# Kernel tuning notes

Measured on AMD Instinct MI355X. Metric: run time of the kernel, lower is better.

The kernel has to match this reference:

```python
import jax, jax.numpy as jnp
import numpy as np

MEM, KEY, VAL, DIN, BS, BQ = 1000, 64, 128, 512, 512, 65536


def setup_inputs() -> dict:
    key = jax.random.key(0)
    ks = jax.random.split(key, 20)

    def lin(k, fan_in, shape):
        return (jax.random.normal(k, shape, jnp.float32) / np.sqrt(fan_in)).astype(jnp.float32)

    return {
        "support_x": jax.random.normal(ks[0], (BS, DIN), jnp.float32),
        "support_y": jax.random.normal(ks[1], (BS, VAL), jnp.float32),
        "query_x": jax.random.normal(ks[2], (BQ, DIN), jnp.float32),
        "query_y": jax.random.normal(ks[3], (BQ, 1), jnp.float32),
        # base model: Linear(DIN -> KEY)
        "base_W": lin(ks[4], DIN, (DIN, KEY)),
        "base_b": jnp.zeros((KEY,), jnp.float32),
        # ExternalMemory projections
        "kp_W": lin(ks[5], KEY, (KEY, KEY)),
        "kp_b": jnp.zeros((KEY,), jnp.float32),
        "vp_W": lin(ks[6], VAL, (VAL, VAL)),
        "vp_b": jnp.zeros((VAL,), jnp.float32),
        # memory buffers (randn keys/values like register_buffer(torch.randn))
        "mem_keys": jax.random.normal(ks[7], (MEM, KEY), jnp.float32),
        "mem_values": jax.random.normal(ks[8], (MEM, VAL), jnp.float32),
        # ages: uniform so top-k picks distinct slots deterministically
        "mem_age": jax.random.uniform(ks[9], (MEM,), jnp.float32),
        # controller MLP: Linear(KEY+VAL,128) ReLU Linear(128,64) ReLU Linear(64,1)
        "c1_W": lin(ks[10], KEY + VAL, (KEY + VAL, 128)),
        "c1_b": jnp.zeros((128,), jnp.float32),
        "c2_W": lin(ks[11], 128, (128, 64)),
        "c2_b": jnp.zeros((64,), jnp.float32),
        "c3_W": lin(ks[12], 64, (64, 1)),
        "c3_b": jnp.zeros((1,), jnp.float32),
    }


def reference(support_x, support_y, query_x, query_y,
              base_W, base_b, kp_W, kp_b, vp_W, vp_b,
              mem_keys, mem_values, mem_age,
              c1_W, c1_b, c2_W, c2_b, c3_W, c3_b):
    # base model features
    support_feat = support_x @ base_W + base_b          # [BS, KEY]
    query_feat = query_x @ base_W + base_b              # [BQ, KEY]

    # --- memory.write(support_feat, support_y) ---
    proj_keys = support_feat @ kp_W + kp_b              # [BS, KEY]
    proj_vals = support_y @ vp_W + vp_b                 # [BS, VAL]
    _, oldest = jax.lax.top_k(mem_age, BS)              # evict oldest BS slots
    new_keys = mem_keys.at[oldest].set(proj_keys)       # [MEM, KEY]
    new_values = mem_values.at[oldest].set(proj_vals)   # [MEM, VAL]

    # --- memory.read(query_feat) ---
    proj_q = query_feat @ kp_W + kp_b                   # [BQ, KEY]
    sims = proj_q @ new_keys.T                          # [BQ, MEM]
    attn = jax.nn.softmax(sims, axis=-1)
    retrieved = attn @ new_values                       # [BQ, VAL]

    # --- controller MLP on [query_feat ; retrieved] ---
    aug = jnp.concatenate([query_feat, retrieved], axis=-1)  # [BQ, KEY+VAL]
    h = jax.nn.relu(aug @ c1_W + c1_b)
    h = jax.nn.relu(h @ c2_W + c2_b)
    query_pred = h @ c3_W + c3_b                        # [BQ, 1]

    meta_loss = jnp.mean((query_pred - query_y) ** 2)
    return meta_loss, query_pred, retrieved
```

## Files before the change

### kernel.cpp

```cpp
#include <hip/hip_runtime.h>

typedef _Float16 h8v __attribute__((ext_vector_type(8)));
typedef _Float16 h4v __attribute__((ext_vector_type(4)));
typedef float    f4v __attribute__((ext_vector_type(4)));

#define MFMA16(a,b,c) __builtin_amdgcn_mfma_f32_16x16x32_f16((a),(b),(c),0,0,0)
#define NEGF (-1e30f)

#define MEM 1000
#define KEY 64
#define VAL 128
#define DIN 512
#define BS  512
#define BQ  65536
#define NCOPY 8


typedef __attribute__((address_space(1))) const unsigned int guint;
typedef __attribute__((address_space(3))) unsigned int luint;

__device__ __forceinline__ void gld16(const _Float16* g, _Float16* l)
{
  __builtin_amdgcn_global_load_lds((guint*)g, (luint*)l, 16, 0, 0);
}

__device__ __forceinline__ h8v cvt8(const float* p)
{
  f4v u = *(const f4v*)p;
  f4v v = *(const f4v*)(p + 4);
  h8v a;
  a[0] = (_Float16)u.x; a[1] = (_Float16)u.y; a[2] = (_Float16)u.z; a[3] = (_Float16)u.w;
  a[4] = (_Float16)v.x; a[5] = (_Float16)v.y; a[6] = (_Float16)v.z; a[7] = (_Float16)v.w;
  return a;
}

__device__ __forceinline__ h8v cvt8nt(const float* p)
{
  f4v u = __builtin_nontemporal_load((const f4v*)p);
  f4v v = __builtin_nontemporal_load((const f4v*)(p + 4));
  h8v a;
  a[0] = (_Float16)u.x; a[1] = (_Float16)u.y; a[2] = (_Float16)u.z; a[3] = (_Float16)u.w;
  a[4] = (_Float16)v.x; a[5] = (_Float16)v.y; a[6] = (_Float16)v.z; a[7] = (_Float16)v.w;
  return a;
}

__global__ void k_prep1(const float* __restrict__ baseW, const float* __restrict__ base_b,
                        const float* __restrict__ kpW, const float* __restrict__ kp_b,
                        const float* __restrict__ vpW, const float* __restrict__ c1W,
                        const float* __restrict__ c2W, const float* __restrict__ age,
                        _Float16* __restrict__ WTf, float* __restrict__ bcomb,
                        _Float16* __restrict__ vpWt, _Float16* __restrict__ c1F,
                        _Float16* __restrict__ c2F, int* __restrict__ ranks,
                        float* __restrict__ out0)
{
  long id = (long)blockIdx.x * 256 + threadIdx.x;
  if (id < 65536) {
    int h = (int)id;
    int j = h & 7, lane = (h >> 3) & 63, KS = (h >> 9) & 15, F = h >> 13;
    int n = F * 16 + (lane & 15);
    int k = KS * 32 + ((lane >> 4) << 3) + j;
    float v;
    if (n < 64) v = baseW[(size_t)k * 64 + n];
    else {
      int nn = n - 64;
      const float* br = baseW + (size_t)k * 64;
      float s = 0.f;
      for (int t = 0; t < 64; ++t) s += br[t] * kpW[t * 64 + nn];
      v = s;
    }
    WTf[h] = (_Float16)v;
  } else if (id < 65664) {
    int i = (int)(id - 65536);
    if (i < 64) bcomb[i] = base_b[i];
    else {
      int n = i - 64;
      float s = kp_b[n];
      for (int t = 0; t < 64; ++t) s += base_b[t] * kpW[t * 64 + n];
      bcomb[i] = s;
    }
  } else if (id < 90240) {
    int h = (int)(id - 65664);
    int j = h & 7, lane = (h >> 3) & 63, KS = (h >> 9) % 6, F = (h >> 9) / 6;
    int n = F * 16 + (lane & 15);
    int k = KS * 32 + ((lane >> 4) << 3) + j;
    c1F[h] = (_Float16)c1W[(size_t)k * 128 + n];
  } else if (id < 98432) {
    int h = (int)(id - 90240);
    int j = h & 7, lane = (h >> 3) & 63, KS = (h >> 9) & 3, F = h >> 11;
    int n = F * 16 + (lane & 15);
    int k = KS * 32 + ((lane >> 4) << 3) + j;
    c2F[h] = (_Float16)c2W[(size_t)k * 64 + n];
  } else if (id < 114816) {
    long i = id - 98432;
    int n = (int)(i >> 7), k = (int)(i & 127);
    vpWt[i] = (_Float16)vpW[(size_t)k * 128 + n];
  } else if (id < 115816) {
    int jx = (int)(id - 114816);
    float aj = age[jx];
    int r = 0;
    for (int i2 = 0; i2 < MEM; ++i2) {
      float ai = age[i2];
      r += (ai > aj) || (ai == aj && i2 < jx);
    }
    ranks[jx] = r;
  } else if (id == 115816) {
    *out0 = 0.f;
  }
}

__global__ __launch_bounds__(64) void k_prep2(
    const float* __restrict__ sx, const float* __restrict__ sy,
    const _Float16* __restrict__ WTf, const float* __restrict__ bcomb,
    const _Float16* __restrict__ vpWt, const float* __restrict__ vp_b,
    float* __restrict__ pkeys, float* __restrict__ pvals)
{
  const int lane = threadIdx.x, quad = lane >> 4, l15 = lane & 15;
  const f4v fz = {0.f, 0.f, 0.f, 0.f};
  if (blockIdx.x < 32) {
    const int m0 = blockIdx.x * 16;
    f4v acc[4];
    #pragma unroll
    for (int f = 0; f < 4; ++f) acc[f] = fz;
    const float* xr = sx + (size_t)(m0 + l15) * DIN;
    #pragma unroll 4
    for (int ks = 0; ks < 16; ++ks) {
      int k0 = ks * 32 + quad * 8;
      h8v a = cvt8(xr + k0);
      #pragma unroll
      for (int f = 0; f < 4; ++f) {
        h8v b = *(const h8v*)(WTf + (size_t)((((4 + f) * 16) + ks) * 64 + lane) * 8);
        acc[f] = MFMA16(a, b, acc[f]);
      }
    }
    #pragma unroll
    for (int f = 0; f < 4; ++f) {
      int col = f * 16 + l15;
      float bb = bcomb[64 + col];
      #pragma unroll
      for (int r = 0; r < 4; ++r)
        pkeys[(size_t)(m0 + quad * 4 + r) * KEY + col] = acc[f][r] + bb;
    }
  } else {
    const int m0 = (blockIdx.x - 32) * 16;
    f4v acc[8];
    #pragma unroll
    for (int f = 0; f < 8; ++f) acc[f] = fz;
    const float* yr = sy + (size_t)(m0 + l15) * VAL;
    #pragma unroll
    for (int ks = 0; ks < 4; ++ks) {
      int k0 = ks * 32 + quad * 8;
      h8v a = cvt8(yr + k0);
      #pragma unroll
      for (int f = 0; f < 8; ++f) {
        h8v b = *(const h8v*)(vpWt + (size_t)(f * 16 + l15) * 128 + k0);
        acc[f] = MFMA16(a, b, acc[f]);
      }
    }
    #pragma unroll
    for (int f = 0; f < 8; ++f) {
      int col = f * 16 + l15;
      float bb = vp_b[col];
      #pragma unroll
      for (int r = 0; r < 4; ++r)
        pvals[(size_t)(m0 + quad * 4 + r) * VAL + col] = acc[f][r] + bb;
    }
  }
}

__global__ void k_prep3(const int* __restrict__ ranks, const float* __restrict__ pk,
                        const float* __restrict__ pv, const float* __restrict__ memK,
                        const float* __restrict__ memV,
                        _Float16* __restrict__ keysF, _Float16* __restrict__ valF,
                        _Float16* __restrict__ WTf, _Float16* __restrict__ c1F,
                        _Float16* __restrict__ c2F)
{
  long id = (long)blockIdx.x * 256 + threadIdx.x;
  if (id < 8L * 65536) {
    int h = (int)(id & 65535);
    int copy = (int)(id >> 16);
    int j = h & 7, lane = (h >> 3) & 63, KS = (h >> 9) & 1, F = h >> 10;
    int n = F * 16 + (lane & 15);
    int k = KS * 32 + ((lane >> 4) << 3) + j;
    float v = 0.f;
    if (n < MEM) {
      int rk = ranks[n];
      v = (rk < BS) ? pk[(size_t)rk * KEY + k] : memK[(size_t)n * KEY + k];
    }
    keysF[(size_t)copy * 65536 + h] = (_Float16)v;
  } else if (id < 8L * 65536 + 8L * 131072) {
    long i = id - 8L * 65536;
    int h = (int)(i & 131071);
    int copy = (int)(i >> 17);
    int j = h & 7, lane = (h >> 3) & 63, KS = (h >> 9) & 31, F = h >> 14;
    int nv = F * 16 + (lane & 15);
    int jm = KS * 32 + ((j >> 2) << 4) + ((lane >> 4) << 2) + (j & 3);
    float v = 0.f;
    if (jm < MEM) {
      int rk = ranks[jm];
      v = (rk < BS) ? pv[(size_t)rk * VAL + nv] : memV[(size_t)jm * VAL + nv];
    }
    valF[(size_t)copy * 131072 + h] = (_Float16)v;
  } else {
    long i = id - (8L * 65536 + 8L * 131072);
    if (i < 7L * 65536) {
      int copy = 1 + (int)(i >> 16); int h = (int)(i & 65535);
      WTf[(size_t)copy * 65536 + h] = WTf[h];
    } else if ((i -= 7L * 65536) < 7L * 24576) {
      int copy = 1 + (int)(i / 24576); int h = (int)(i % 24576);
      c1F[(size_t)copy * 24576 + h] = c1F[h];
    } else if ((i -= 7L * 24576) < 7L * 8192) {
      int copy = 1 + (int)(i >> 13); int h = (int)(i & 8191);
      c2F[(size_t)copy * 8192 + h] = c2F[h];
    }
  }
}

__global__ __launch_bounds__(512, 4) void k_fused(
    const float* __restrict__ qx, const float* __restrict__ qy,
    const _Float16* __restrict__ WTf_, const float* __restrict__ bcomb,
    const float* __restrict__ c1_b, const float* __restrict__ c2_b,
    const float* __restrict__ c3W, const float* __restrict__ c3b,
    const _Float16* __restrict__ c1F_, const _Float16* __restrict__ c2F_,
    const _Float16* __restrict__ keysF_, const _Float16* __restrict__ valF_,
    float* __restrict__ dout)
{
  __shared__ __align__(16) char smem[65536];
  _Float16* const Wq0 = (_Float16*)smem;
  _Float16* const Wq1 = (_Float16*)(smem + 32768);
  _Float16* const K0 = (_Float16*)smem;
  _Float16* const K1 = (_Float16*)(smem + 8192);
  _Float16* const V0 = (_Float16*)(smem + 16384);
  _Float16* const V1 = (_Float16*)(smem + 32768);

  const int tid  = threadIdx.x;
  const int wid  = tid >> 6;
  const int lane = tid & 63;
  const int quad = lane >> 4;
  const int l15  = lane & 15;

  const int cpy  = blockIdx.x & 7;
  const int rot  = (blockIdx.x >> 3) & 15;
  const int qrot = (blockIdx.x >> 1) & 3;
  const _Float16* const WTf   = WTf_   + (size_t)cpy * 65536;
  const _Float16* const c1F   = c1F_   + (size_t)cpy * 24576;
  const _Float16* const c2F   = c2F_   + (size_t)cpy * 8192;
  const _Float16* const keysF = keysF_ + (size_t)cpy * 65536;
  const _Float16* const valF  = valF_  + (size_t)cpy * 131072;

  _Float16* const qstash = (_Float16*)(smem + 49152 + wid * 2048);
  _Float16* const P_s  = (_Float16*)(smem + wid * 6656);
  _Float16* const h2_s = P_s + 2176;

  const int tile = blockIdx.x * 8 + wid;
  const int q0   = tile * 16;

  float* out_pred = dout + 1;
  float* out_ret  = dout + 1 + BQ;
  const f4v fz = {0.f, 0.f, 0.f, 0.f};

  #pragma unroll
  for (int i = 0; i < 4; ++i) {
    const int t = wid * 4 + i;
    const int f = t >> 2, ksq = t & 3;
    gld16(WTf + (size_t)(f * 16 + qrot * 4 + ksq) * 512 + lane * 8, Wq0 + t * 512);
  }
  asm volatile("s_waitcnt vmcnt(0)" ::: "memory");
  __syncthreads();

  f4v acc[8];
  #pragma unroll
  for (int f = 0; f < 8; ++f) acc[f] = fz;
  const float* xr = qx + (size_t)(q0 + l15) * DIN;

  #pragma unroll
  for (int q = 0; q < 4; ++q) {
    const int qe = (q + qrot) & 3;
    _Float16* const Wb = (q & 1) ? Wq1 : Wq0;
    _Float16* const Wn = (q & 1) ? Wq0 : Wq1;
    if (q < 3) {
      const int qn = (q + 1 + qrot) & 3;
      #pragma unroll
      for (int i = 0; i < 4; ++i) {
        const int t = wid * 4 + i;
        const int f = t >> 2, ksq = t & 3;
        gld16(WTf + (size_t)(f * 16 + qn * 4 + ksq) * 512 + lane * 8,
              Wn + t * 512);
      }
    }
    #pragma unroll
    for (int ksq = 0; ksq < 4; ++ksq) {
      const int ks = qe * 4 + ksq;
      h8v a = cvt8nt(xr + ks * 32 + quad * 8);
      #pragma unroll
      for (int f = 0; f < 8; ++f) {
        h8v b = *(const h8v*)(Wb + (size_t)((f * 4 + ksq) * 64 + lane) * 8);
        acc[f] = MFMA16(a, b, acc[f]);
      }
    }
    asm volatile("s_waitcnt vmcnt(0)" ::: "memory");
    __syncthreads();
  }

  _Float16* tbuf = (_Float16*)(smem + wid * 4352);
  h8v pq0, pq1;
  {
    #pragma unroll
    for (int f = 0; f < 8; ++f) {
      float bb = bcomb[f * 16 + l15];
      #pragma unroll
      for (int r = 0; r < 4; ++r)
        tbuf[(quad * 4 + r) * 136 + f * 16 + l15] = (_Float16)(acc[f][r] + bb);
    }
    h8v qf0 = *(const h8v*)&tbuf[l15 * 136 +  0 + quad * 8];
    h8v qf1 = *(const h8v*)&tbuf[l15 * 136 + 32 + quad * 8];
    pq0 = *(const h8v*)&tbuf[l15 * 136 + 64 + quad * 8];
    pq1 = *(const h8v*)&tbuf[l15 * 136 + 96 + quad * 8];
    *(h8v*)&qstash[0 * 512 + lane * 8] = qf0;
    *(h8v*)&qstash[1 * 512 + lane * 8] = qf1;
  }
  __syncthreads();

  #pragma unroll
  for (int i = 0; i < 3; ++i) {
    const int t = wid * 3 + i;
    if (t < 8) gld16(keysF + (size_t)(rot * 8 + t) * 512 + lane * 8, K0 + t * 512);
    else {
      const int tv = t - 8;
      gld16(valF + (size_t)((tv >> 1) * 32 + rot * 2 + (tv & 1)) * 512 + lane * 8,
            V0 + tv * 512);
    }
  }
  asm volatile("s_waitcnt vmcnt(0)" ::: "memory");
  __syncthreads();

  float rm = NEGF, rl = 0.f;
  f4v O[8];
  #pragma unroll
  for (int v = 0; v < 8; ++v) O[v] = fz;

  #pragma unroll 1
  for (int c = 0; c < 16; ++c) {
    const int ce  = (c + rot) & 15;
    const int cur = c & 1;
    _Float16* const Kc = cur ? K1 : K0;
    _Float16* const Vc = cur ? V1 : V0;
    _Float16* const Kn = cur ? K0 : K1;
    _Float16* const Vn = cur ? V0 : V1;

    if (c < 15) {
      const int ne = (c + 1 + rot) & 15;
      #pragma unroll
      for (int i = 0; i < 3; ++i) {
        const int t = wid * 3 + i;
        if (t < 8)
          gld16(keysF + (size_t)(ne * 8 + t) * 512 + lane * 8, Kn + t * 512);
        else {
          const int tv = t - 8;
          gld16(valF + (size_t)((tv >> 1) * 32 + ne * 2 + (tv & 1)) * 512 + lane * 8,
                Vn + tv * 512);
        }
      }
    }

    f4v S[4];
    #pragma unroll
    for (int f = 0; f < 4; ++f) S[f] = fz;
    #pragma unroll
    for (int f = 0; f < 4; ++f) {
      h8v b0 = *(const h8v*)(Kc + (size_t)(f * 2 + 0) * 512 + lane * 8);
      h8v b1 = *(const h8v*)(Kc + (size_t)(f * 2 + 1) * 512 + lane * 8);
      S[f] = MFMA16(b0, pq0, S[f]);
      S[f] = MFMA16(b1, pq1, S[f]);
    }

    float cm = NEGF;
    #pragma unroll
    for (int f = 0; f < 4; ++f) {
      const int sb = ce * 64 + f * 16 + quad * 4;
      #pragma unroll
      for (int r = 0; r < 4; ++r) {
        float s = (sb + r < MEM) ? S[f][r] : NEGF;
        S[f][r] = s;
        cm = fmaxf(cm, s);
      }
    }
    cm = fmaxf(cm, __shfl_xor(cm, 16));
    cm = fmaxf(cm, __shfl_xor(cm, 32));
    if (__any(cm > rm)) {
      float mn = fmaxf(rm, cm);
      float al = __expf(rm - mn);
      rm = mn;
      float alO[4];
      #pragma unroll
      for (int r = 0; r < 4; ++r) alO[r] = __shfl(al, quad * 4 + r);
      #pragma unroll
      for (int v = 0; v < 8; ++v)
        #pragma unroll
        for (int r = 0; r < 4; ++r) O[v][r] *= alO[r];
      rl *= al;
    }
    float psl = 0.f;
    #pragma unroll
    for (int f = 0; f < 4; ++f)
      #pragma unroll
      for (int r = 0; r < 4; ++r) {
        float p = __expf(S[f][r] - rm);
        S[f][r] = p;
        psl += p;
      }
    rl += psl;

    #pragma unroll
    for (int ks2 = 0; ks2 < 2; ++ks2) {
      h8v a;
      #pragma unroll
      for (int e = 0; e < 4; ++e) {
        a[e]     = (_Float16)S[2 * ks2][e];
        a[e + 4] = (_Float16)S[2 * ks2 + 1][e];
      }
      #pragma unroll
      for (int v = 0; v < 8; ++v) {
        h8v b = *(const h8v*)(Vc + (size_t)(v * 2 + ks2) * 512 + lane * 8);
        O[v] = MFMA16(a, b, O[v]);
      }
    }

    asm volatile("s_waitcnt vmcnt(0)" ::: "memory");
    __syncthreads();
  }

  rl += __shfl_xor(rl, 16); rl += __shfl_xor(rl, 32);
  float rlO[4];
  #pragma unroll
  for (int r = 0; r < 4; ++r) rlO[r] = __shfl(rl, quad * 4 + r);

  h8v qf0 = *(const h8v*)&qstash[0 * 512 + lane * 8];
  h8v qf1 = *(const h8v*)&qstash[1 * 512 + lane * 8];
  __syncthreads();

  #pragma unroll
  for (int v = 0; v < 8; ++v)
    #pragma unroll
    for (int r = 0; r < 4; ++r)
      P_s[(quad * 4 + r) * 136 + v * 16 + l15] = (_Float16)(O[v][r] / rlO[r]);

  #pragma unroll
  for (int it = 0; it < 8; ++it) {
    int flat = it * 256 + lane * 4;
    int row = flat >> 7, col = flat & 127;
    h4v t = *(const h4v*)&P_s[row * 136 + col];
    f4v o;
    o.x = (float)t[0]; o.y = (float)t[1]; o.z = (float)t[2]; o.w = (float)t[3];
    __builtin_nontemporal_store(o, (f4v*)(out_ret + (size_t)q0 * VAL + flat));
  }

  {
    f4v H[8];
    #pragma unroll
    for (int f = 0; f < 8; ++f) H[f] = fz;
    #pragma unroll
    for (int ks = 0; ks < 6; ++ks) {
      const int k0 = ks * 32;
      h8v a = (ks == 0) ? qf0 : (ks == 1) ? qf1
               : *(const h8v*)&P_s[l15 * 136 + (k0 - 64) + quad * 8];
      #pragma unroll
      for (int f = 0; f < 8; ++f) {
        h8v b = *(const h8v*)(c1F + (size_t)(f * 6 + ks) * 512 + lane * 8);
        H[f] = MFMA16(a, b, H[f]);
      }
    }
    #pragma unroll
    for (int f = 0; f < 8; ++f) {
      float bb = c1_b[f * 16 + l15];
      #pragma unroll
      for (int r = 0; r < 4; ++r)
        P_s[(quad * 4 + r) * 136 + f * 16 + l15] =
            (_Float16)fmaxf(0.f, H[f][r] + bb);
    }
  }

  {
    f4v G[4];
    #pragma unroll
    for (int f = 0; f < 4; ++f) G[f] = fz;
    #pragma unroll
    for (int ks = 0; ks < 4; ++ks) {
      h8v a = *(const h8v*)&P_s[l15 * 136 + ks * 32 + quad * 8];
      #pragma unroll
      for (int f = 0; f < 4; ++f) {
        h8v b = *(const h8v*)(c2F + (size_t)(f * 4 + ks) * 512 + lane * 8);
        G[f] = MFMA16(a, b, G[f]);
      }
    }
    #pragma unroll
    for (int f = 0; f < 4; ++f) {
      float bb = c2_b[f * 16 + l15];
      #pragma unroll
      for (int r = 0; r < 4; ++r)
        h2_s[(quad * 4 + r) * 72 + f * 16 + l15] =
            (_Float16)fmaxf(0.f, G[f][r] + bb);
    }
  }

  float lsum;
  {
    const int prow = lane >> 2, pj = lane & 3;
    float s = 0.f;
    #pragma unroll
    for (int k = 0; k < 16; ++k) {
      int kk = pj * 16 + k;
      s += (float)h2_s[prow * 72 + kk] * c3W[kk];
    }
    s += __shfl_xor(s, 1);
    s += __shfl_xor(s, 2);
    float pred = s + c3b[0];
    float diff = pred - qy[q0 + prow];
    if (pj == 0) out_pred[q0 + prow] = pred;
    lsum = diff * diff;
  }
  #pragma unroll
  for (int m = 1; m < 64; m <<= 1) lsum += __shfl_xor(lsum, m);
  if (lane == 0) atomicAdd(dout, lsum * (1.0f / (4.0f * (float)BQ)));
}

extern "C" void kernel_launch(void* const* d_in, const int* in_sizes, int n_in,
                              void* d_out, int out_size, void* d_ws, size_t ws_size,
                              hipStream_t stream)
{
  const float* support_x = (const float*)d_in[0];
  const float* support_y = (const float*)d_in[1];
  const float* query_x   = (const float*)d_in[2];
  const float* query_y   = (const float*)d_in[3];
  const float* base_W    = (const float*)d_in[4];
  const float* base_b    = (const float*)d_in[5];
  const float* kp_W      = (const float*)d_in[6];
  const float* kp_b      = (const float*)d_in[7];
  const float* vp_W      = (const float*)d_in[8];
  const float* vp_b      = (const float*)d_in[9];
  const float* mem_keys  = (const float*)d_in[10];
  const float* mem_vals  = (const float*)d_in[11];
  const float* mem_age   = (const float*)d_in[12];
  const float* c1_W      = (const float*)d_in[13];
  const float* c1_b      = (const float*)d_in[14];
  const float* c2_W      = (const float*)d_in[15];
  const float* c2_b      = (const float*)d_in[16];
  const float* c3_W      = (const float*)d_in[17];
  const float* c3_b      = (const float*)d_in[18];

  char* w = (char*)d_ws;
  _Float16* WTf   = (_Float16*)(w + 0);
  _Float16* c1F   = (_Float16*)(w + 1048576);
  _Float16* c2F   = (_Float16*)(w + 1441792);
  _Float16* keysF = (_Float16*)(w + 1572864);
  _Float16* valF  = (_Float16*)(w + 2621440);
  _Float16* vpWt  = (_Float16*)(w + 4718592);
  float*    bcomb = (float*)   (w + 4751360);
  int*      ranks = (int*)     (w + 4751872);
  float*    pkeys = (float*)   (w + 4755968);
  float*    pvals = (float*)   (w + 4887040);

  float* out = (float*)d_out;

  hipLaunchKernelGGL(k_prep1, dim3(453), dim3(256), 0, stream,
                     base_W, base_b, kp_W, kp_b, vp_W, c1_W, c2_W, mem_age,
                     WTf, bcomb, vpWt, c1F, c2F, ranks, out);
  hipLaunchKernelGGL(k_prep2, dim3(64), dim3(64), 0, stream,
                     support_x, support_y, WTf, bcomb, vpWt, vp_b, pkeys, pvals);
  hipLaunchKernelGGL(k_prep3, dim3(8832), dim3(256), 0, stream,
                     ranks, pkeys, pvals, mem_keys, mem_vals, keysF, valF,
                     WTf, c1F, c2F);
  hipLaunchKernelGGL(k_fused, dim3(BQ / 128), dim3(512), 0, stream,
                     query_x, query_y, WTf, bcomb, c1_b, c2_b, c3_W, c3_b,
                     c1F, c2F, keysF, valF, out);
}
```

Before: 364.4 us.

## Stage full weights and keys in LDS, load values directly from global

```diff
diff --git a/kernel.cpp b/kernel.cpp
--- a/kernel.cpp
+++ b/kernel.cpp
@@ -215,7 +215,7 @@
   }
 }
 
-__global__ __launch_bounds__(512, 4) void k_fused(
+__global__ __launch_bounds__(512, 2) void k_fused(
     const float* __restrict__ qx, const float* __restrict__ qy,
     const _Float16* __restrict__ WTf_, const float* __restrict__ bcomb,
     const float* __restrict__ c1_b, const float* __restrict__ c2_b,
@@ -224,13 +224,8 @@
     const _Float16* __restrict__ keysF_, const _Float16* __restrict__ valF_,
     float* __restrict__ dout)
 {
-  __shared__ __align__(16) char smem[65536];
-  _Float16* const Wq0 = (_Float16*)smem;
-  _Float16* const Wq1 = (_Float16*)(smem + 32768);
-  _Float16* const K0 = (_Float16*)smem;
-  _Float16* const K1 = (_Float16*)(smem + 8192);
-  _Float16* const V0 = (_Float16*)(smem + 16384);
-  _Float16* const V1 = (_Float16*)(smem + 32768);
+  __shared__ __align__(16) char smem[147456];
+  _Float16* const smh = (_Float16*)smem;
 
   const int tid  = threadIdx.x;
   const int wid  = tid >> 6;
@@ -240,15 +235,14 @@
 
   const int cpy  = blockIdx.x & 7;
   const int rot  = (blockIdx.x >> 3) & 15;
-  const int qrot = (blockIdx.x >> 1) & 3;
   const _Float16* const WTf   = WTf_   + (size_t)cpy * 65536;
   const _Float16* const c1F   = c1F_   + (size_t)cpy * 24576;
   const _Float16* const c2F   = c2F_   + (size_t)cpy * 8192;
   const _Float16* const keysF = keysF_ + (size_t)cpy * 65536;
   const _Float16* const valF  = valF_  + (size_t)cpy * 131072;
 
-  _Float16* const qstash = (_Float16*)(smem + 49152 + wid * 2048);
-  _Float16* const P_s  = (_Float16*)(smem + wid * 6656);
+  _Float16* const qstash = smh + 65536 + wid * 1024;
+  _Float16* const P_s  = smh + wid * 3328;
   _Float16* const h2_s = P_s + 2176;
 
   const int tile = blockIdx.x * 8 + wid;
@@ -259,10 +253,9 @@
   const f4v fz = {0.f, 0.f, 0.f, 0.f};
 
   #pragma unroll
-  for (int i = 0; i < 4; ++i) {
-    const int t = wid * 4 + i;
-    const int f = t >> 2, ksq = t & 3;
-    gld16(WTf + (size_t)(f * 16 + qrot * 4 + ksq) * 512 + lane * 8, Wq0 + t * 512);
+  for (int i = 0; i < 16; ++i) {
+    const int t = wid * 16 + i;
+    gld16(WTf + (size_t)t * 512 + lane * 8, smh + t * 512);
   }
   asm volatile("s_waitcnt vmcnt(0)" ::: "memory");
   __syncthreads();
@@ -272,36 +265,19 @@
   for (int f = 0; f < 8; ++f) acc[f] = fz;
   const float* xr = qx + (size_t)(q0 + l15) * DIN;
 
-  #pragma unroll
-  for (int q = 0; q < 4; ++q) {
-    const int qe = (q + qrot) & 3;
-    _Float16* const Wb = (q & 1) ? Wq1 : Wq0;
-    _Float16* const Wn = (q & 1) ? Wq0 : Wq1;
-    if (q < 3) {
-      const int qn = (q + 1 + qrot) & 3;
-      #pragma unroll
-      for (int i = 0; i < 4; ++i) {
-        const int t = wid * 4 + i;
-        const int f = t >> 2, ksq = t & 3;
-        gld16(WTf + (size_t)(f * 16 + qn * 4 + ksq) * 512 + lane * 8,
-              Wn + t * 512);
-      }
-    }
-    #pragma unroll
-    for (int ksq = 0; ksq < 4; ++ksq) {
-      const int ks = qe * 4 + ksq;
-      h8v a = cvt8nt(xr + ks * 32 + quad * 8);
-      #pragma unroll
-      for (int f = 0; f < 8; ++f) {
-        h8v b = *(const h8v*)(Wb + (size_t)((f * 4 + ksq) * 64 + lane) * 8);
-        acc[f] = MFMA16(a, b, acc[f]);
-      }
-    }
-    asm volatile("s_waitcnt vmcnt(0)" ::: "memory");
-    __syncthreads();
-  }
-
-  _Float16* tbuf = (_Float16*)(smem + wid * 4352);
+  #pragma unroll 4
+  for (int ks = 0; ks < 16; ++ks) {
+    const int k0 = ks * 32 + quad * 8;
+    h8v a = cvt8nt(xr + k0);
+    #pragma unroll
+    for (int f = 0; f < 8; ++f) {
+      h8v b = *(const h8v*)(smh + (size_t)((f * 16 + ks) * 64 + lane) * 8);
+      acc[f] = MFMA16(a, b, acc[f]);
+    }
+  }
+  __syncthreads();
+
+  _Float16* tbuf = smh + wid * 2176;
   h8v pq0, pq1;
   {
     #pragma unroll
@@ -321,14 +297,9 @@
   __syncthreads();
 
   #pragma unroll
-  for (int i = 0; i < 3; ++i) {
-    const int t = wid * 3 + i;
-    if (t < 8) gld16(keysF + (size_t)(rot * 8 + t) * 512 + lane * 8, K0 + t * 512);
-    else {
-      const int tv = t - 8;
-      gld16(valF + (size_t)((tv >> 1) * 32 + rot * 2 + (tv & 1)) * 512 + lane * 8,
-            V0 + tv * 512);
-    }
+  for (int i = 0; i < 16; ++i) {
+    const int t = wid * 16 + i;
+    gld16(keysF + (size_t)t * 512 + lane * 8, smh + t * 512);
   }
   asm volatile("s_waitcnt vmcnt(0)" ::: "memory");
   __syncthreads();
@@ -340,49 +311,44 @@
 
   #pragma unroll 1
   for (int c = 0; c < 16; ++c) {
-    const int ce  = (c + rot) & 15;
-    const int cur = c & 1;
-    _Float16* const Kc = cur ? K1 : K0;
-    _Float16* const Vc = cur ? V1 : V0;
-    _Float16* const Kn = cur ? K0 : K1;
-    _Float16* const Vn = cur ? V0 : V1;
-
-    if (c < 15) {
-      const int ne = (c + 1 + rot) & 15;
-      #pragma unroll
-      for (int i = 0; i < 3; ++i) {
-        const int t = wid * 3 + i;
-        if (t < 8)
-          gld16(keysF + (size_t)(ne * 8 + t) * 512 + lane * 8, Kn + t * 512);
-        else {
-          const int tv = t - 8;
-          gld16(valF + (size_t)((tv >> 1) * 32 + ne * 2 + (tv & 1)) * 512 + lane * 8,
-                Vn + tv * 512);
-        }
-      }
-    }
+    const int ce = (c + rot) & 15;
+
+    h8v VA[16];
+    #pragma unroll
+    for (int v = 0; v < 8; ++v)
+      #pragma unroll
+      for (int ks2 = 0; ks2 < 2; ++ks2)
+        VA[v * 2 + ks2] =
+            *(const h8v*)(valF + (size_t)(v * 32 + ce * 2 + ks2) * 512 + lane * 8);
 
     f4v S[4];
     #pragma unroll
     for (int f = 0; f < 4; ++f) S[f] = fz;
     #pragma unroll
     for (int f = 0; f < 4; ++f) {
-      h8v b0 = *(const h8v*)(Kc + (size_t)(f * 2 + 0) * 512 + lane * 8);
-      h8v b1 = *(const h8v*)(Kc + (size_t)(f * 2 + 1) * 512 + lane * 8);
+      h8v b0 = *(const h8v*)(smh + (size_t)(ce * 8 + f * 2 + 0) * 512 + lane * 8);
+      h8v b1 = *(const h8v*)(smh + (size_t)(ce * 8 + f * 2 + 1) * 512 + lane * 8);
       S[f] = MFMA16(b0, pq0, S[f]);
       S[f] = MFMA16(b1, pq1, S[f]);
     }
 
     float cm = NEGF;
-    #pragma unroll
-    for (int f = 0; f < 4; ++f) {
-      const int sb = ce * 64 + f * 16 + quad * 4;
-      #pragma unroll
-      for (int r = 0; r < 4; ++r) {
-        float s = (sb + r < MEM) ? S[f][r] : NEGF;
-        S[f][r] = s;
-        cm = fmaxf(cm, s);
-      }
+    if (ce == 15) {
+      #pragma unroll
+      for (int f = 0; f < 4; ++f) {
+        const int sb = 960 + f * 16 + quad * 4;
+        #pragma unroll
+        for (int r = 0; r < 4; ++r) {
+          float s = (sb + r < MEM) ? S[f][r] : NEGF;
+          S[f][r] = s;
+          cm = fmaxf(cm, s);
+        }
+      }
+    } else {
+      #pragma unroll
+      for (int f = 0; f < 4; ++f)
+        #pragma unroll
+        for (int r = 0; r < 4; ++r) cm = fmaxf(cm, S[f][r]);
     }
     cm = fmaxf(cm, __shfl_xor(cm, 16));
     cm = fmaxf(cm, __shfl_xor(cm, 32));
@@ -419,15 +385,11 @@
         a[e + 4] = (_Float16)S[2 * ks2 + 1][e];
       }
       #pragma unroll
-      for (int v = 0; v < 8; ++v) {
-        h8v b = *(const h8v*)(Vc + (size_t)(v * 2 + ks2) * 512 + lane * 8);
-        O[v] = MFMA16(a, b, O[v]);
-      }
-    }
-
-    asm volatile("s_waitcnt vmcnt(0)" ::: "memory");
-    __syncthreads();
-  }
+      for (int v = 0; v < 8; ++v)
+        O[v] = MFMA16(a, VA[v * 2 + ks2], O[v]);
+    }
+  }
+  __syncthreads();
 
   rl += __shfl_xor(rl, 16); rl += __shfl_xor(rl, 32);
   float rlO[4];
@@ -436,7 +398,6 @@
 
   h8v qf0 = *(const h8v*)&qstash[0 * 512 + lane * 8];
   h8v qf1 = *(const h8v*)&qstash[1 * 512 + lane * 8];
-  __syncthreads();
 
   #pragma unroll
   for (int v = 0; v < 8; ++v)
```

Result: no change. 367.0 us (+0.7%).
